# Kernel tuning notes

Measured on AMD Instinct MI355X. Metric: run time of the kernel, lower is better.

## Reference

```python
import jax, jax.numpy as jnp
import numpy as np
import math

B, S, D, H = 1, 2048, 2048, 16
DH = D // H  # 128
HALF = DH // 2  # 64


def setup_inputs() -> dict:
    key = jax.random.key(0)
    ks = jax.random.split(key, 6)
    x = jax.random.normal(ks[0], (B, S, D), dtype=jnp.float32)
    # rotary frequencies: freqs_cis = exp(i * t * theta), theta_j = 10000^{-2j/DH}
    inv_freq = 1.0 / (10000.0 ** (np.arange(0, DH, 2, dtype=np.float32) / DH))  # [HALF]
    t = np.arange(S, dtype=np.float32)
    angles = np.outer(t, inv_freq)  # [S, HALF]
    freqs_cos = jnp.asarray(np.cos(angles), dtype=jnp.float32)
    freqs_sin = jnp.asarray(np.sin(angles), dtype=jnp.float32)
    # additive causal mask [1,1,S,S]
    mask = jnp.triu(jnp.full((S, S), -1e9, dtype=jnp.float32), k=1)[None, None]
    scale = 0.02
    wq = jax.random.normal(ks[1], (D, D), dtype=jnp.float32) * scale
    wk = jax.random.normal(ks[2], (D, D), dtype=jnp.float32) * scale
    wv = jax.random.normal(ks[3], (D, D), dtype=jnp.float32) * scale
    wo = jax.random.normal(ks[4], (D, D), dtype=jnp.float32) * scale
    return {"x": x, "freqs_cos": freqs_cos, "freqs_sin": freqs_sin, "mask": mask,
            "wq": wq, "wk": wk, "wv": wv, "wo": wo, "start_pos": 0}


def _apply_rope(t, cos, sin):
    # t: [B,S,H,DH]; cos/sin: [S,HALF] broadcast as [1,S,1,HALF]
    tr = t.reshape(*t.shape[:-1], HALF, 2)
    even, odd = tr[..., 0], tr[..., 1]
    c = cos[None, :, None, :]
    s = sin[None, :, None, :]
    out_even = even * c - odd * s
    out_odd = even * s + odd * c
    return jnp.stack([out_even, out_odd], axis=-1).reshape(t.shape)


def reference(x, freqs_cos, freqs_sin, mask, wq, wk, wv, wo, start_pos):
    bsz, seqlen, _ = x.shape
    q = (x @ wq.T).reshape(bsz, seqlen, H, DH)
    k = (x @ wk.T).reshape(bsz, seqlen, H, DH)
    v = (x @ wv.T).reshape(bsz, seqlen, H, DH)
    q = _apply_rope(q, freqs_cos, freqs_sin)
    k = _apply_rope(k, freqs_cos, freqs_sin)
    q = q.transpose(0, 2, 1, 3)  # [B,H,S,DH]
    k = k.transpose(0, 2, 1, 3)
    v = v.transpose(0, 2, 1, 3)
    scores = jnp.einsum('bhqd,bhkd->bhqk', q, k) / math.sqrt(DH) + mask
    probs = jax.nn.softmax(scores, axis=-1)
    out = jnp.einsum('bhqk,bhkd->bhqd', probs, v)  # [B,H,S,DH]
    # faithful to original: transpose(2,3) then view(bsz, seqlen, dim)
    out = out.transpose(0, 1, 3, 2).reshape(bsz, seqlen, D)
    return out @ wo.T
```

## Files before the change

kernel.cpp:

```cpp
#include <hip/hip_runtime.h>

typedef unsigned short u16;
typedef unsigned int   u32;
typedef short  short8   __attribute__((ext_vector_type(8)));
typedef float  floatx4  __attribute__((ext_vector_type(4)));
typedef u16    ushortx2 __attribute__((ext_vector_type(2)));
typedef u16    ushortx4 __attribute__((ext_vector_type(4)));

__device__ __forceinline__ float bf2f(u16 u) {
  union { u32 i; float f; } v; v.i = ((u32)u) << 16; return v.f;
}
__device__ __forceinline__ u16 f2bf(float x) {
  union { float f; u32 i; } v; v.f = x;
  u32 r = v.i + 0x7FFFu + ((v.i >> 16) & 1u);
  return (u16)(r >> 16);
}

#if __has_builtin(__builtin_amdgcn_exp2f)
#define EXP2F(x) __builtin_amdgcn_exp2f(x)
#else
#define EXP2F(x) __exp2f(x)
#endif

#define GLOAD_LDS16(gptr, lptr)                                                   \
  __builtin_amdgcn_global_load_lds(                                               \
      (const __attribute__((address_space(1))) void*)(gptr),                      \
      (__attribute__((address_space(3))) void*)(lptr), 16, 0, 0)

#define WAITV(n) asm volatile("s_waitcnt vmcnt(" #n ")" ::: "memory")
#define WAITL    asm volatile("s_waitcnt lgkmcnt(0)" ::: "memory")
#define BAR      __builtin_amdgcn_s_barrier()

__global__ __launch_bounds__(256) void cvt_all(
    const floatx4* __restrict__ x,  const floatx4* __restrict__ wq,
    const floatx4* __restrict__ wk, const floatx4* __restrict__ wv,
    const floatx4* __restrict__ wo,
    ushortx4* __restrict__ xb, ushortx4* __restrict__ wqkv,
    ushortx4* __restrict__ wob) {
  int i = blockIdx.x * 256 + threadIdx.x;
  const floatx4* in; ushortx4* out;
  switch (blockIdx.y) {
    case 0:  in = x;  out = xb; break;
    case 1:  in = wq; out = wqkv; break;
    case 2:  in = wk; out = wqkv + (size_t)1048576; break;
    case 3:  in = wv; out = wqkv + (size_t)2097152; break;
    default: in = wo; out = wob; break;
  }
  floatx4 v = in[i];
  ushortx4 o;
  o.x = f2bf(v.x); o.y = f2bf(v.y); o.z = f2bf(v.z); o.w = f2bf(v.w);
  out[i] = o;
}

__global__ __launch_bounds__(512, 2) void gemm256_bt(
    const u16* __restrict__ A, const u16* __restrict__ B, u16* __restrict__ C,
    int N, int K, int lda, int ldb, int ldc) {
  const int cpx = gridDim.x >> 3;
  const int wg = ((int)blockIdx.x & 7) * cpx + ((int)blockIdx.x >> 3);
  const int ntn = N / 192;
  const int m0 = (wg / ntn) << 8;
  const int n0 = (wg % ntn) * 192;

  __shared__ __align__(16) u16 As[2][256][64];
  __shared__ __align__(16) u16 Bs[2][192][64];

  const int t = threadIdx.x;
  const int lane = t & 63;
  const int wave = t >> 6;
  const int wr = wave >> 2;
  const int wc = wave & 3;
  const int quad = lane >> 4;
  const int mrow = lane & 15;
  const int sw = mrow & 7;

  const int srow = lane >> 3;
  const int gso  = ((lane & 7) ^ srow) << 3;

  const u16* gA = A + (size_t)(m0 + (wave << 3) + srow) * lda + gso;
  const u16* gB = B + (size_t)(n0 + (wave << 3) + srow) * ldb + gso;

  floatx4 acc[8][3] = {};
  short8 afr[4][2], bfr[3][2];

  const int NT = K >> 6;

#define ST_A(nb, h, kt)                                                        \
  do {                                                                         \
    GLOAD_LDS16(gA + (size_t)((h) * 128) * lda + ((kt) << 6),                  \
                &As[nb][(h) * 128 + (wave << 3)][0]);                          \
    GLOAD_LDS16(gA + (size_t)((h) * 128 + 64) * lda + ((kt) << 6),             \
                &As[nb][(h) * 128 + 64 + (wave << 3)][0]);                     \
  } while (0)
#define ST_B1(nb, c, kt)                                                       \
  do {                                                                         \
    GLOAD_LDS16(gB + (size_t)((c) * 64) * ldb + ((kt) << 6),                   \
                &Bs[nb][(c) * 64 + (wave << 3)][0]);                           \
  } while (0)

#define LDA4(bf, base_row)                                                     \
  do {                                                                         \
    _Pragma("unroll") for (int i_ = 0; i_ < 4; i_++)                           \
      _Pragma("unroll") for (int kk_ = 0; kk_ < 2; kk_++)                      \
        afr[i_][kk_] = *(const short8*)&As[bf][(base_row) + (i_ << 4) + mrow]  \
                            [(((kk_ << 2) | quad) ^ sw) << 3];                 \
  } while (0)
#define LDB1(bf, j)                                                            \
  do {                                                                         \
    _Pragma("unroll") for (int kk_ = 0; kk_ < 2; kk_++)                        \
      bfr[j][kk_] = *(const short8*)&Bs[bf][(j) * 64 + (wc << 4) + mrow]       \
          [(((kk_ << 2) | quad) ^ sw) << 3];                                   \
  } while (0)
#define MMQ8(ilo, j)                                                           \
  do {                                                                         \
    __builtin_amdgcn_s_setprio(1);                                             \
    _Pragma("unroll") for (int kk_ = 0; kk_ < 2; kk_++)                        \
      _Pragma("unroll") for (int i_ = 0; i_ < 4; i_++)                         \
        acc[(ilo) + i_][j] = __builtin_amdgcn_mfma_f32_16x16x32_bf16(          \
            afr[i_][kk_], bfr[j][kk_], acc[(ilo) + i_][j], 0, 0, 0);           \
    __builtin_amdgcn_s_setprio(0);                                             \
  } while (0)

  ST_A(0, 0, 0); ST_B1(0, 0, 0); ST_B1(0, 1, 0); ST_B1(0, 2, 0); ST_A(0, 1, 0);
  WAITV(3);
  BAR;

  for (int kt = 0; kt < NT - 1; kt++) {
    const int bf = kt & 1, nb = bf ^ 1;
    LDA4(bf, (wr << 6));
    LDB1(bf, 0);
    LDB1(bf, 1);
    ST_A(nb, 0, kt + 1);
    ST_B1(nb, 0, kt + 1);
    WAITV(3);
    BAR;
    MMQ8(0, 0);
    MMQ8(0, 1);
    LDB1(bf, 2);
    ST_B1(nb, 1, kt + 1);
    ST_B1(nb, 2, kt + 1);
    BAR;
    MMQ8(0, 2);
    LDA4(bf, 128 + (wr << 6));
    MMQ8(4, 0);
    ST_A(nb, 1, kt + 1);
    WAITV(3);
    BAR;
    MMQ8(4, 1);
    MMQ8(4, 2);
  }
  {
    const int bf = (NT - 1) & 1;
    LDA4(bf, (wr << 6));
    LDB1(bf, 0);
    LDB1(bf, 1);
    WAITV(0);
    BAR;
    MMQ8(0, 0);
    MMQ8(0, 1);
    LDB1(bf, 2);
    BAR;
    MMQ8(0, 2);
    LDA4(bf, 128 + (wr << 6));
    MMQ8(4, 0);
    BAR;
    MMQ8(4, 1);
    MMQ8(4, 2);
  }

#pragma unroll
  for (int i = 0; i < 8; i++) {
    int row0 = m0 + ((i >= 4) ? 128 : 0) + (wr << 6) + ((i & 3) << 4) + (quad << 2);
#pragma unroll
    for (int j = 0; j < 3; j++) {
      int col = n0 + j * 64 + (wc << 4) + mrow;
#pragma unroll
      for (int r = 0; r < 4; r++)
        C[(size_t)(row0 + r) * ldc + col] = f2bf(acc[i][j][r]);
    }
  }
#undef ST_A
#undef ST_B1
#undef LDA4
#undef LDB1
#undef MMQ8
}

__global__ __launch_bounds__(256, 2) void gemm_out(
    const u16* __restrict__ A, const u16* __restrict__ B,
    float* __restrict__ C) {
  const int wg = ((int)blockIdx.x & 7) * 32 + ((int)blockIdx.x >> 3);
  const int m0 = (wg >> 4) << 7;
  const int n0 = (wg & 15) << 7;

  __shared__ __align__(16) u16 As[2][128][64];
  __shared__ __align__(16) u16 Bs[2][128][64];

  const int t = threadIdx.x;
  const int lane = t & 63;
  const int wave = t >> 6;
  const int wr = wave >> 1;
  const int wc = wave & 1;
  const int quad = lane >> 4;
  const int mrow = lane & 15;
  const int sw = mrow & 7;

  const int srow = lane >> 3;
  const int gso  = ((lane & 7) ^ srow) << 3;

  const u16* gA = A + (size_t)(m0 + (wave << 3) + srow) * 2048 + gso;
  const u16* gB = B + (size_t)(n0 + (wave << 3) + srow) * 2048 + gso;

  floatx4 acc[4][4] = {};
  short8 afr[4][2], bfr[4][2];

  const int NT = 32;

#define OST_A(nb, p, kt)                                                       \
  GLOAD_LDS16(gA + (size_t)((p) * 32) * 2048 + ((kt) << 6),                    \
              &As[nb][(p) * 32 + (wave << 3)][0])
#define OST_B(nb, p, kt)                                                       \
  GLOAD_LDS16(gB + (size_t)((p) * 32) * 2048 + ((kt) << 6),                    \
              &Bs[nb][(p) * 32 + (wave << 3)][0])

#define OLDA(bf)                                                               \
  do {                                                                         \
    _Pragma("unroll") for (int i_ = 0; i_ < 4; i_++)                           \
      _Pragma("unroll") for (int kk_ = 0; kk_ < 2; kk_++)                      \
        afr[i_][kk_] = *(const short8*)&As[bf][(wr << 6) + (i_ << 4) + mrow]   \
                            [(((kk_ << 2) | quad) ^ sw) << 3];                 \
  } while (0)
#define OLDB2(bf, jlo)                                                         \
  do {                                                                         \
    _Pragma("unroll") for (int j_ = 0; j_ < 2; j_++)                           \
      _Pragma("unroll") for (int kk_ = 0; kk_ < 2; kk_++)                      \
        bfr[(jlo) + j_][kk_] =                                                 \
            *(const short8*)&Bs[bf][(wc << 6) + (((jlo) + j_) << 4) + mrow]    \
                [(((kk_ << 2) | quad) ^ sw) << 3];                             \
  } while (0)
#define OMM16(jlo)                                                             \
  do {                                                                         \
    __builtin_amdgcn_s_setprio(1);                                             \
    _Pragma("unroll") for (int kk_ = 0; kk_ < 2; kk_++)                        \
      _Pragma("unroll") for (int i_ = 0; i_ < 4; i_++)                         \
        _Pragma("unroll") for (int j_ = 0; j_ < 2; j_++)                       \
          acc[i_][(jlo) + j_] = __builtin_amdgcn_mfma_f32_16x16x32_bf16(       \
              afr[i_][kk_], bfr[(jlo) + j_][kk_], acc[i_][(jlo) + j_], 0, 0, 0);\
    __builtin_amdgcn_s_setprio(0);                                             \
  } while (0)

  OST_A(0, 0, 0); OST_A(0, 1, 0); OST_A(0, 2, 0); OST_A(0, 3, 0);
  OST_B(0, 0, 0); OST_B(0, 2, 0); OST_B(0, 1, 0); OST_B(0, 3, 0);
  WAITV(2);
  BAR;

  for (int kt = 0; kt < NT - 1; kt++) {
    const int bf = kt & 1, nb = bf ^ 1;
    OLDA(bf);
    OLDB2(bf, 0);
    OST_A(nb, 0, kt + 1); OST_A(nb, 1, kt + 1);
    OST_A(nb, 2, kt + 1); OST_A(nb, 3, kt + 1);
    OST_B(nb, 0, kt + 1); OST_B(nb, 2, kt + 1);
    WAITV(6);
    BAR;
    OMM16(0);
    OLDB2(bf, 2);
    OST_B(nb, 1, kt + 1); OST_B(nb, 3, kt + 1);
    WAITV(2);
    BAR;
    OMM16(2);
  }
  {
    const int bf = (NT - 1) & 1;
    OLDA(bf);
    OLDB2(bf, 0);
    WAITV(0);
    BAR;
    OMM16(0);
    OLDB2(bf, 2);
    OMM16(2);
  }

#pragma unroll
  for (int i = 0; i < 4; i++) {
    int row0 = m0 + (wr << 6) + (i << 4) + (quad << 2);
#pragma unroll
    for (int j = 0; j < 4; j++) {
      int col = n0 + (wc << 6) + (j << 4) + mrow;
#pragma unroll
      for (int r = 0; r < 4; r++)
        C[(size_t)(row0 + r) * 2048 + col] = acc[i][j][r];
    }
  }
#undef OST_A
#undef OST_B
#undef OLDA
#undef OLDB2
#undef OMM16
}

__global__ __launch_bounds__(256) void rope_trans(
    u16* __restrict__ qkv, const float* __restrict__ cs,
    const float* __restrict__ sn, u16* __restrict__ vt) {
  __shared__ u16 tile[64][68];
  const int bx = blockIdx.x;
  if (bx < 16384) {
    const int isK = bx >> 13;
    int idx = (bx & 8191) * 256 + threadIdx.x;
    int p = idx & 63;
    int h = (idx >> 6) & 15;
    int s = idx >> 10;
    float c  = cs[(s << 6) | p];
    float si = sn[(s << 6) | p];
    float scale = isK ? 1.0f : 0.12751743f;
    size_t off = (size_t)s * 6144 + (isK ? 2048 : 0) + (h << 7) + (p << 1);
    ushortx2 eo = *(ushortx2*)(qkv + off);
    float e = bf2f(eo.x), o = bf2f(eo.y);
    ushortx2 r;
    r.x = f2bf((e * c - o * si) * scale);
    r.y = f2bf((e * si + o * c) * scale);
    *(ushortx2*)(qkv + off) = r;
  } else {
    const int b = bx - 16384;
    const u16* src = qkv + 4096;
    const int d0 = (b & 31) << 6;
    const int s0 = (b >> 5) << 6;
    const int tx = (threadIdx.x & 15) << 2;
    const int ty = threadIdx.x >> 4;
#pragma unroll
    for (int rr = 0; rr < 64; rr += 16) {
      ushortx4 v = *(const ushortx4*)(src + (size_t)(s0 + ty + rr) * 6144 + d0 + tx);
      *(ushortx4*)&tile[ty + rr][tx] = v;
    }
    __syncthreads();
#pragma unroll
    for (int rr = 0; rr < 64; rr += 16) {
      int r = ty + rr;
      ushortx4 o;
      o.x = tile[tx + 0][r]; o.y = tile[tx + 1][r];
      o.z = tile[tx + 2][r]; o.w = tile[tx + 3][r];
      *(ushortx4*)(vt + (size_t)(d0 + r) * 2048 + s0 + tx) = o;
    }
  }
}

__global__ __launch_bounds__(512, 1) void flash_attn(
    const u16* __restrict__ QKVp, const u16* __restrict__ VTp,
    u16* __restrict__ ATp) {
  const int bid = (int)blockIdx.x;
  const int h   = bid & 15;
  const int g   = bid >> 4;

  __shared__ __align__(16) u16 Ks[2][128][128];
  __shared__ __align__(16) u16 Vs[2][128][128];
  __shared__ __align__(16) u16 Ps[64][128];

  const int t = threadIdx.x;
  const int lane = t & 63;
  const int wave = t >> 6;
  const int quad = lane >> 4;
  const int mrow = lane & 15;
  const int sw   = mrow & 7;
  const int wmS = (wave & 1) << 5;
  const int wnS = (wave >> 1) << 5;
  const int wmV = (wave >> 1) << 5;
  const int wnP = (wave & 1) << 5;

  const int r4  = lane >> 4;
  const int seg = lane & 15;
  const int c0 = ((seg ^ r4) << 3);
  const int c4 = ((seg ^ (r4 + 4)) << 3);

  const u16* kbase = QKVp + 2048 + (h << 7);
  const u16* vbase = VTp + (size_t)(h << 7) * 2048;

#define STAGE_K(nb, kt)                                                        \
  do {                                                                         \
    int rr0_ = wave << 4;                                                      \
    _Pragma("unroll") for (int ii_ = 0; ii_ < 4; ii_++) {                      \
      int rr_ = rr0_ + (ii_ << 2);                                             \
      GLOAD_LDS16(kbase + (size_t)(((kt) << 7) + rr_ + r4) * 6144 +            \
                      ((ii_ & 1) ? c4 : c0),                                   \
                  &Ks[nb][rr_][0]);                                            \
    }                                                                          \
  } while (0)
#define STAGE_V(nb, kt)                                                        \
  do {                                                                         \
    int rr0_ = wave << 4;                                                      \
    _Pragma("unroll") for (int ii_ = 0; ii_ < 4; ii_++) {                      \
      int rr_ = rr0_ + (ii_ << 2);                                             \
      GLOAD_LDS16(vbase + (size_t)(rr_ + r4) * 2048 + ((kt) << 7) +            \
                      ((ii_ & 1) ? c4 : c0),                                   \
                  &Vs[nb][rr_][0]);                                            \
    }                                                                          \
  } while (0)

  const short8 ones = {0x3F80, 0x3F80, 0x3F80, 0x3F80,
                       0x3F80, 0x3F80, 0x3F80, 0x3F80};
  const float C2 = 23.083120654223414f;

  for (int pass = 0; pass < 2; pass++) {
    const int qsub  = pass ? g : 31 - g;
    const int q0    = qsub << 6;
    const int ktmax = qsub >> 1;
    const u16* qbase = QKVp + (size_t)q0 * 6144 + (h << 7);

    short8 aq[2][4];
#pragma unroll
    for (int i = 0; i < 2; i++)
#pragma unroll
      for (int kk = 0; kk < 4; kk++)
        aq[i][kk] = *(const short8*)(qbase +
                        (size_t)(wmS + (i << 4) + mrow) * 6144 +
                        (kk << 5) + (quad << 3));

    floatx4 Oa[2][2] = {};
    floatx4 Oa1[2] = {};

    STAGE_K(0, 0);
    STAGE_V(0, 0);
    WAITV(4);
    BAR;

    for (int kt = 0; kt <= ktmax; kt++) {
      const int b = kt & 1, nb = b ^ 1;

      floatx4 sa[2][2] = {};
#pragma unroll
      for (int kk = 0; kk < 4; kk++) {
        short8 bk[2];
#pragma unroll
        for (int j = 0; j < 2; j++)
          bk[j] = *(const short8*)&Ks[b][wnS + (j << 4) + mrow]
                      [(((kk << 2) | quad) ^ sw) << 3];
        __builtin_amdgcn_s_setprio(1);
#pragma unroll
        for (int i = 0; i < 2; i++)
#pragma unroll
          for (int j = 0; j < 2; j++)
            sa[i][j] = __builtin_amdgcn_mfma_f32_16x16x32_bf16(
                aq[i][kk], bk[j], sa[i][j], 0, 0, 0);
        __builtin_amdgcn_s_setprio(0);
      }

      if (kt < ktmax) {
        STAGE_K(nb, kt + 1);
        STAGE_V(nb, kt + 1);
      }

      if (kt == ktmax) {
#pragma unroll
        for (int i = 0; i < 2; i++)
#pragma unroll
          for (int j = 0; j < 2; j++)
#pragma unroll
            for (int r = 0; r < 4; r++) {
              int ql = q0 + wmS + (i << 4) + (quad << 2) + r;
              int sl = (kt << 7) + wnS + (j << 4) + mrow;
              if (sl > ql) sa[i][j][r] = -1e30f;
            }
      }
#pragma unroll
      for (int i = 0; i < 2; i++)
#pragma unroll
        for (int j = 0; j < 2; j++)
#pragma unroll
          for (int r = 0; r < 4; r++) {
            int row = wmS + (i << 4) + (quad << 2) + r;
            int col = wnS + (j << 4) + mrow;
            Ps[row][((((col >> 3) ^ (row & 7)) << 3) | (col & 7))] =
                f2bf(EXP2F(sa[i][j][r] - C2));
          }
      WAITL;
      if (kt < ktmax) WAITV(8);
      else            WAITV(0);
      BAR;

#pragma unroll
      for (int kk = 0; kk < 4; kk++) {
        short8 av[2], bp[2];
#pragma unroll
        for (int i = 0; i < 2; i++)
          av[i] = *(const short8*)&Vs[b][wmV + (i << 4) + mrow]
                      [(((kk << 2) | quad) ^ sw) << 3];
#pragma unroll
        for (int j = 0; j < 2; j++)
          bp[j] = *(const short8*)&Ps[wnP + (j << 4) + mrow]
                      [(((kk << 2) | quad) ^ sw) << 3];
        __builtin_amdgcn_s_setprio(1);
#pragma unroll
        for (int i = 0; i < 2; i++)
#pragma unroll
          for (int j = 0; j < 2; j++)
            Oa[i][j] = __builtin_amdgcn_mfma_f32_16x16x32_bf16(
                av[i], bp[j], Oa[i][j], 0, 0, 0);
#pragma unroll
        for (int j = 0; j < 2; j++)
          Oa1[j] = __builtin_amdgcn_mfma_f32_16x16x32_bf16(
              ones, bp[j], Oa1[j], 0, 0, 0);
        __builtin_amdgcn_s_setprio(0);
      }
      if (kt < ktmax) WAITV(4);
      BAR;
    }

    float linv[2];
#pragma unroll
    for (int j = 0; j < 2; j++) linv[j] = 1.f / Oa1[j][0];
#pragma unroll
    for (int i = 0; i < 2; i++) {
      int drow = (h << 7) + wmV + (i << 4) + (quad << 2);
#pragma unroll
      for (int j = 0; j < 2; j++) {
        int col = q0 + wnP + (j << 4) + mrow;
#pragma unroll
        for (int r = 0; r < 4; r++)
          ATp[(size_t)(drow + r) * 2048 + col] = f2bf(Oa[i][j][r] * linv[j]);
      }
    }
  }
#undef STAGE_K
#undef STAGE_V
}

extern "C" void kernel_launch(void* const* d_in, const int* in_sizes, int n_in,
                              void* d_out, int out_size, void* d_ws, size_t ws_size,
                              hipStream_t stream) {
  const float* x  = (const float*)d_in[0];
  const float* fc = (const float*)d_in[1];
  const float* fs = (const float*)d_in[2];
  const float* wq = (const float*)d_in[4];
  const float* wk = (const float*)d_in[5];
  const float* wv = (const float*)d_in[6];
  const float* wo = (const float*)d_in[7];
  float* out = (float*)d_out;

  char* ws = (char*)d_ws;
  const size_t MB = 1024 * 1024;
  u16*   XB   = (u16*)(ws + 0 * MB);
  u16*   WQKV = (u16*)(ws + 8 * MB);
  u16*   WOb  = (u16*)(ws + 32 * MB);
  u16*   QKV  = (u16*)(ws + 40 * MB);
  u16*   VT   = (u16*)(ws + 64 * MB);
  u16*   AT   = (u16*)(ws + 72 * MB);

  dim3 blk(256);
  cvt_all<<<dim3(4096, 5), blk, 0, stream>>>(
      (const floatx4*)x, (const floatx4*)wq, (const floatx4*)wk,
      (const floatx4*)wv, (const floatx4*)wo,
      (ushortx4*)XB, (ushortx4*)WQKV, (ushortx4*)WOb);

  gemm256_bt<<<dim3(256), dim3(512), 0, stream>>>(XB, WQKV, QKV,
                                                  6144, 2048, 2048, 2048, 6144);

  rope_trans<<<dim3(17408), blk, 0, stream>>>(QKV, fc, fs, VT);

  flash_attn<<<dim3(256), dim3(512), 0, stream>>>(QKV, VT, AT);

  gemm_out<<<dim3(256), blk, 0, stream>>>(AT, WOb, out);
}
```

Baseline: 266.3 us.

## Software-pipeline LDS fragment reads across K iterations in QKV GEMM

Restructures the QKV GEMM main loop so that the A first-half and B columns 0-1 fragments for the next K tile are read from LDS at the end of the current iteration, using ping-pong register sets and a loop unrolled by two. The goal is to hide LDS read latency behind the MFMAs of the current tile instead of stalling at the start of each iteration. In exchange it raises VGPR pressure with the extra fragment buffers, which could hurt occupancy under launch_bounds(256,2). It also assumes NT is even for the final peeled iteration.

Result: no change. 268.7 us (+0.9%).

```diff
diff --git a/kernel.cpp b/kernel.cpp
--- a/kernel.cpp
+++ b/kernel.cpp
@@ -80,7 +80,9 @@
   const u16* gB = B + (size_t)(n0 + (wave << 3) + srow) * ldb + gso;
 
   floatx4 acc[8][3] = {};
-  short8 afr[4][2], bfr[3][2];
+  short8 afh0[4][2], afh1[4][2];
+  short8 b01E[2][2], b01O[2][2];
+  short8 bfr2[2];
 
   const int NT = K >> 6;
 
@@ -97,74 +99,91 @@
                 &Bs[nb][(c) * 64 + (wave << 3)][0]);                           \
   } while (0)
 
-#define LDA4(bf, base_row)                                                     \
+#define RD_AH0(bf)                                                             \
   do {                                                                         \
     _Pragma("unroll") for (int i_ = 0; i_ < 4; i_++)                           \
-      _Pragma("unroll") for (int kk_ = 0; kk_ < 2; kk_++)                      \
-        afr[i_][kk_] = *(const short8*)&As[bf][(base_row) + (i_ << 4) + mrow]  \
-                            [(((kk_ << 2) | quad) ^ sw) << 3];                 \
-  } while (0)
-#define LDB1(bf, j)                                                            \
-  do {                                                                         \
-    _Pragma("unroll") for (int kk_ = 0; kk_ < 2; kk_++)                        \
-      bfr[j][kk_] = *(const short8*)&Bs[bf][(j) * 64 + (wc << 4) + mrow]       \
-          [(((kk_ << 2) | quad) ^ sw) << 3];                                   \
-  } while (0)
-#define MMQ8(ilo, j)                                                           \
+      _Pragma("unroll") for (int k_ = 0; k_ < 2; k_++)                         \
+        afh0[i_][k_] = *(const short8*)&As[bf][(wr << 6) + (i_ << 4) + mrow]   \
+                            [(((k_ << 2) | quad) ^ sw) << 3];                  \
+  } while (0)
+#define RD_AH1(bf)                                                             \
+  do {                                                                         \
+    _Pragma("unroll") for (int i_ = 0; i_ < 4; i_++)                           \
+      _Pragma("unroll") for (int k_ = 0; k_ < 2; k_++)                         \
+        afh1[i_][k_] = *(const short8*)&As[bf][128 + (wr << 6) + (i_ << 4) + mrow] \
+                            [(((k_ << 2) | quad) ^ sw) << 3];                  \
+  } while (0)
+#define RD_B01(bf, DST)                                                        \
+  do {                                                                         \
+    _Pragma("unroll") for (int j_ = 0; j_ < 2; j_++)                           \
+      _Pragma("unroll") for (int k_ = 0; k_ < 2; k_++)                         \
+        DST[j_][k_] = *(const short8*)&Bs[bf][j_ * 64 + (wc << 4) + mrow]      \
+                          [(((k_ << 2) | quad) ^ sw) << 3];                    \
+  } while (0)
+#define RD_B2(bf)                                                              \
+  do {                                                                         \
+    _Pragma("unroll") for (int k_ = 0; k_ < 2; k_++)                           \
+      bfr2[k_] = *(const short8*)&Bs[bf][128 + (wc << 4) + mrow]               \
+                     [(((k_ << 2) | quad) ^ sw) << 3];                         \
+  } while (0)
+
+#define MM8(AF, BF2, ilo, j)                                                   \
   do {                                                                         \
     __builtin_amdgcn_s_setprio(1);                                             \
-    _Pragma("unroll") for (int kk_ = 0; kk_ < 2; kk_++)                        \
+    _Pragma("unroll") for (int k_ = 0; k_ < 2; k_++)                           \
       _Pragma("unroll") for (int i_ = 0; i_ < 4; i_++)                         \
         acc[(ilo) + i_][j] = __builtin_amdgcn_mfma_f32_16x16x32_bf16(          \
-            afr[i_][kk_], bfr[j][kk_], acc[(ilo) + i_][j], 0, 0, 0);           \
+            AF[i_][k_], BF2[k_], acc[(ilo) + i_][j], 0, 0, 0);                 \
     __builtin_amdgcn_s_setprio(0);                                             \
+  } while (0)
+
+#define BODY(kt, bf, nb, BC, BN)                                               \
+  do {                                                                         \
+                                                                       \
+    ST_A(nb, 0, (kt) + 1); ST_B1(nb, 0, (kt) + 1);                             \
+    WAITV(3);                                                                  \
+    BAR;                                                                       \
+    RD_B2(bf);                                                                 \
+    MM8(afh0, BC[0], 0, 0);                                                    \
+    MM8(afh0, BC[1], 0, 1);                                                    \
+                                                                       \
+    ST_B1(nb, 1, (kt) + 1); ST_B1(nb, 2, (kt) + 1);                            \
+    BAR;                                                                       \
+    RD_AH1(bf);                                                                \
+    MM8(afh0, bfr2, 0, 2);                                                     \
+    MM8(afh1, BC[0], 4, 0);                                                    \
+                                                                       \
+    ST_A(nb, 1, (kt) + 1);                                                     \
+    WAITV(3);                                                                  \
+    BAR;                                                                       \
+    RD_AH0(nb); RD_B01(nb, BN);                                                \
+    MM8(afh1, BC[1], 4, 1);                                                    \
+    MM8(afh1, bfr2, 4, 2);                                                     \
   } while (0)
 
   ST_A(0, 0, 0); ST_B1(0, 0, 0); ST_B1(0, 1, 0); ST_B1(0, 2, 0); ST_A(0, 1, 0);
   WAITV(3);
   BAR;
-
-  for (int kt = 0; kt < NT - 1; kt++) {
-    const int bf = kt & 1, nb = bf ^ 1;
-    LDA4(bf, (wr << 6));
-    LDB1(bf, 0);
-    LDB1(bf, 1);
-    ST_A(nb, 0, kt + 1);
-    ST_B1(nb, 0, kt + 1);
-    WAITV(3);
-    BAR;
-    MMQ8(0, 0);
-    MMQ8(0, 1);
-    LDB1(bf, 2);
-    ST_B1(nb, 1, kt + 1);
-    ST_B1(nb, 2, kt + 1);
-    BAR;
-    MMQ8(0, 2);
-    LDA4(bf, 128 + (wr << 6));
-    MMQ8(4, 0);
-    ST_A(nb, 1, kt + 1);
-    WAITV(3);
-    BAR;
-    MMQ8(4, 1);
-    MMQ8(4, 2);
-  }
+  RD_AH0(0); RD_B01(0, b01E);
+
+#pragma unroll 1
+  for (int kt = 0; kt + 2 < NT; kt += 2) {
+    BODY(kt, 0, 1, b01E, b01O);
+    BODY(kt + 1, 1, 0, b01O, b01E);
+  }
+  BODY(NT - 2, 0, 1, b01E, b01O);
+
   {
-    const int bf = (NT - 1) & 1;
-    LDA4(bf, (wr << 6));
-    LDB1(bf, 0);
-    LDB1(bf, 1);
     WAITV(0);
     BAR;
-    MMQ8(0, 0);
-    MMQ8(0, 1);
-    LDB1(bf, 2);
-    BAR;
-    MMQ8(0, 2);
-    LDA4(bf, 128 + (wr << 6));
-    MMQ8(4, 0);
-    BAR;
-    MMQ8(4, 1);
-    MMQ8(4, 2);
+    RD_B2(1);
+    MM8(afh0, b01O[0], 0, 0);
+    MM8(afh0, b01O[1], 0, 1);
+    RD_AH1(1);
+    MM8(afh0, bfr2, 0, 2);
+    MM8(afh1, b01O[0], 4, 0);
+    MM8(afh1, b01O[1], 4, 1);
+    MM8(afh1, bfr2, 4, 2);
   }
 
 #pragma unroll
@@ -180,9 +199,12 @@
   }
 #undef ST_A
 #undef ST_B1
-#undef LDA4
-#undef LDB1
-#undef MMQ8
+#undef RD_AH0
+#undef RD_AH1
+#undef RD_B01
+#undef RD_B2
+#undef MM8
+#undef BODY
 }
 
 __global__ __launch_bounds__(256, 2) void gemm_out(
```
